# Performance work log

Measured on AMD Instinct MI355X. Metric: run time of the kernel, lower is better.

The kernel has to match this reference:

```python
import jax, jax.numpy as jnp
import numpy as np

B, C, D, H, W, K = 2, 192, 48, 48, 48, 7
EPS_LN = 1e-6
EPS_GRN = 1e-6


def setup_inputs() -> dict:
    key = jax.random.key(0)
    ks = jax.random.split(key, 8)
    sc = 0.02
    return {
        "x": jax.random.normal(ks[0], (B, C, D, H, W), jnp.float32),
        # depthwise conv kernel in DHWIO layout: [K,K,K,1,C] (torch weight [C,1,K,K,K])
        "conv_w": jax.random.normal(ks[1], (K, K, K, 1, C), jnp.float32) * sc,
        "conv_b": jnp.zeros((C,), jnp.float32),
        "ln_g": jnp.ones((C,), jnp.float32),
        "ln_b": jnp.zeros((C,), jnp.float32),
        "w1": jax.random.normal(ks[2], (C, 4 * C), jnp.float32) * sc,
        "b1": jnp.zeros((4 * C,), jnp.float32),
        "grn_gamma": jax.random.normal(ks[3], (4 * C,), jnp.float32) * sc,
        "grn_beta": jax.random.normal(ks[4], (4 * C,), jnp.float32) * sc,
        "w2": jax.random.normal(ks[5], (4 * C, C), jnp.float32) * sc,
        "b2": jnp.zeros((C,), jnp.float32),
    }


def reference(x, conv_w, conv_b, ln_g, ln_b, w1, b1, grn_gamma, grn_beta, w2, b2):
    c = x.shape[1]
    # NCDHW -> NDHWC (channels-last, as Permute([0,2,3,4,1]) after the conv)
    xc = jnp.transpose(x, (0, 2, 3, 4, 1))
    # depthwise conv3d, kernel 7, pad 3 (SAME for stride 1)
    y = jax.lax.conv_general_dilated(
        xc, conv_w, window_strides=(1, 1, 1), padding="SAME",
        dimension_numbers=("NDHWC", "DHWIO", "NDHWC"),
        feature_group_count=c,
    ) + conv_b
    # LayerNorm over channel dim, eps=1e-6 (biased variance, like torch)
    mu = jnp.mean(y, axis=-1, keepdims=True)
    var = jnp.mean(jnp.square(y - mu), axis=-1, keepdims=True)
    y = (y - mu) * jax.lax.rsqrt(var + EPS_LN) * ln_g + ln_b
    # MLP up + exact GELU
    y = jax.nn.gelu(y @ w1 + b1, approximate=False)
    # GRN: global L2 over spatial dims per channel
    gx = jnp.sqrt(jnp.sum(y * y, axis=(1, 2, 3), keepdims=True))  # [B,1,1,1,4C]
    nx = gx / (jnp.mean(gx, axis=-1, keepdims=True) + EPS_GRN)
    y = grn_gamma * (y * nx) + grn_beta + y
    # MLP down, permute back, residual
    y = y @ w2 + b2
    return jnp.transpose(y, (0, 4, 1, 2, 3)) + x
```

## Files before the change

### kernel.cpp

```cpp
#include <hip/hip_runtime.h>
#include <math.h>

#define Bn 2
#define Cn 192
#define Dn 48
#define Hn 48
#define Wn 48
#define C4 768
#define DHW (Dn*Hn*Wn)
#define CDHW ((long)Cn*DHW)

typedef __attribute__((ext_vector_type(8))) short bf16x8;
typedef __attribute__((ext_vector_type(4))) float f32x4;

__device__ inline float bf2f(unsigned short u) {
    union { float f; unsigned int i; } v; v.i = ((unsigned int)u) << 16; return v.f;
}
__device__ inline unsigned short f2bf(float f) {
    union { float f; unsigned int i; } v; v.f = f;
    unsigned int r = v.i + 0x7FFFu + ((v.i >> 16) & 1u);
    return (unsigned short)(r >> 16);
}
__device__ inline float blo(unsigned int u) {
    union { unsigned int i; float f; } v; v.i = u << 16; return v.f;
}
__device__ inline float bhi(unsigned int u) {
    union { unsigned int i; float f; } v; v.i = u & 0xffff0000u; return v.f;
}
__device__ inline unsigned int cvtpk_bf16(float lo, float hi) {
    unsigned int r;
    asm("v_cvt_pk_bf16_f32 %0, %1, %2" : "=v"(r) : "v"(lo), "v"(hi));
    return r;
}
__device__ inline float gelu_tanh(float v) {
    float u = v * fmaf(0.0356774081f, v * v, 0.7978845608f);
    float a = fabsf(u);
    float t = __expf(-2.0f * a);
    float th = (1.0f - t) / (1.0f + t);
    th = copysignf(th, u);
    return 0.5f * v * (1.0f + th);
}

__global__ __launch_bounds__(256)
void xpad_k(const float* __restrict__ x, unsigned short* __restrict__ xbf)
{
    int u = blockIdx.x * 256 + threadIdx.x;
    int j = u & 7;
    int row = u >> 3;
    unsigned short* orow = xbf + ((size_t)row << 6);
    uint4 o = {0u, 0u, 0u, 0u};
    if (j >= 1 && j <= 6) {
        const float* xr = x + (size_t)row * 48 + (8 * j - 8);
        float4 a = *(const float4*)xr;
        float4 b = *(const float4*)(xr + 4);
        o.x = cvtpk_bf16(a.x, a.y); o.y = cvtpk_bf16(a.z, a.w);
        o.z = cvtpk_bf16(b.x, b.y); o.w = cvtpk_bf16(b.z, b.w);
    }
    *(uint4*)(orow + 8 * j) = o;
}

__global__ __launch_bounds__(256)
void btoep_k(const float* __restrict__ cw, unsigned short* __restrict__ btp)
{
    int idx = blockIdx.x * 256 + threadIdx.x;
    int lane = idx & 63;
    int t = idx >> 6;
    int kdkh = t % 49, c = t / 49;
    int n = lane & 15, g = lane >> 4;
    unsigned short v[8];
#pragma unroll
    for (int j = 0; j < 8; ++j) {
        int kw = 8 * g + j - n - 5;
        v[j] = (kw >= 0 && kw <= 6) ? f2bf(cw[(kdkh * 7 + kw) * Cn + c])
                                    : (unsigned short)0;
    }
    *(uint4*)(btp + (size_t)idx * 8) = *(uint4*)v;
}

#define CTD 16
#define CHD (CTD+6)
#define CHH 22

__global__ __launch_bounds__(128)
void conv_dw(const unsigned short* __restrict__ xbf, const unsigned short* __restrict__ btp,
             const float* __restrict__ cb, unsigned short* __restrict__ yc)
{
    __shared__ unsigned int xt[CHD * CHH * 16];
    int c = blockIdx.y;
    int s = blockIdx.x;
    int wt = s % 3, ht = (s / 3) % 3, dt = s / 9;
    int d0 = dt * 16, h0 = ht * 16, w0 = wt * 16;
    int tid = threadIdx.x;

    const unsigned short* xc = xbf + ((size_t)c * 2304 << 6);
    for (int u = tid; u < CHD * CHH * 4; u += 128) {
        int g = u & 3, r2 = u >> 2;
        int hh2 = r2 % CHH, dd = r2 / CHH;
        int gd = d0 - 3 + dd, gh = h0 - 3 + hh2;
        uint4 v = {0u, 0u, 0u, 0u};
        if ((unsigned)gd < 48u && (unsigned)gh < 48u)
            v = *(const uint4*)(xc + (((size_t)gd * 48 + gh) << 6) + w0 + 8 * g);
        *(uint4*)&xt[(r2 << 4) + ((g ^ (r2 & 3)) << 2)] = v;
    }
    __syncthreads();

    int lane = tid & 63, wv = tid >> 6;
    int lr = lane & 15, g = lane >> 4;
    float bias = cb[c];
    f32x4 acc[8];
#pragma unroll
    for (int t = 0; t < 8; ++t) acc[t] = (f32x4){bias, bias, bias, bias};

    const unsigned short* bchan = btp + (size_t)c * 49 * 512;
    const unsigned short* xt16 = (const unsigned short*)xt;

    for (int kh = 0; kh < 7; ++kh) {
        bf16x8 Bf[7];
#pragma unroll
        for (int kd = 0; kd < 7; ++kd)
            Bf[kd] = *(const bf16x8*)(bchan + (size_t)((kd * 7 + kh) * 64 + lane) * 8);
#pragma unroll
        for (int p = 0; p < 14; ++p) {
            int r2 = (8 * wv + p) * CHH + kh + lr;
            bf16x8 Af = *(const bf16x8*)(xt16 + (r2 << 5) + ((g ^ (r2 & 3)) << 3));
#pragma unroll
            for (int kd = 0; kd < 7; ++kd) {
                int t = p - kd;
                if (t < 0 || t > 7) continue;
                acc[t] = __builtin_amdgcn_mfma_f32_16x16x32_bf16(Af, Bf[kd], acc[t], 0, 0, 0);
            }
        }
    }

    unsigned short* yb = yc + (long)c * DHW;
#pragma unroll
    for (int t = 0; t < 8; ++t) {
        int d = d0 + 8 * wv + t;
#pragma unroll
        for (int i = 0; i < 4; ++i) {
            int h = h0 + g * 4 + i;
            yb[((long)d * 48 + h) * 48 + w0 + lr] = f2bf(acc[t][i]);
        }
    }
}

__global__ __launch_bounds__(256)
void ln_kernel(const unsigned short* __restrict__ yc, const float* __restrict__ g,
               const float* __restrict__ lb, unsigned short* __restrict__ y1)
{
    __shared__ float tile[Cn * Wn];
    __shared__ float qs1[4][48], qs2[4][48];
    __shared__ float mu_s[Wn], rs_s[Wn];
    int dh = blockIdx.x;
    long rowbase = (long)dh * Wn;
    for (int l = threadIdx.x; l < Cn * 24; l += 256) {
        int c = l / 24, wp = l % 24;
        unsigned int u = *(const unsigned int*)&yc[rowbase + (long)c * DHW + wp * 2];
        tile[c * Wn + wp * 2]     = blo(u);
        tile[c * Wn + wp * 2 + 1] = bhi(u);
    }
    __syncthreads();
    if (threadIdx.x < 192) {
        int w = threadIdx.x >> 2, q = threadIdx.x & 3;
        float s1 = 0.f, s2 = 0.f;
        for (int cc = 0; cc < 48; ++cc) {
            float v = tile[(cc * 4 + q) * Wn + w];
            s1 += v; s2 = fmaf(v, v, s2);
        }
        qs1[q][w] = s1; qs2[q][w] = s2;
    }
    __syncthreads();
    if (threadIdx.x < 48) {
        int w = threadIdx.x;
        float s1 = qs1[0][w] + qs1[1][w] + qs1[2][w] + qs1[3][w];
        float s2 = qs2[0][w] + qs2[1][w] + qs2[2][w] + qs2[3][w];
        float mu = s1 * (1.0f / Cn);
        float var = s2 * (1.0f / Cn) - mu * mu;
        mu_s[w] = mu;
        rs_s[w] = rsqrtf(var + 1e-6f);
    }
    __syncthreads();
    long obase = (long)dh * Wn * Cn;
    for (int l = threadIdx.x; l < Cn * Wn; l += 256) {
        int w = l / Cn, c = l % Cn;
        float val = (tile[c * Wn + w] - mu_s[w]) * rs_s[w] * g[c] + lb[c];
        y1[obase + l] = f2bf(val);
    }
}

__global__ __launch_bounds__(256)
void wtrans(const float* __restrict__ W, unsigned short* __restrict__ Wt, int K, int N)
{
    int idx = blockIdx.x * 256 + threadIdx.x;
    if (idx >= K * N) return;
    int n = idx / K, k = idx % K;
    Wt[idx] = f2bf(W[(long)k * N + n]);
}

__global__ __launch_bounds__(256)
void wscale(const float* __restrict__ W2, const float* __restrict__ gx2,
            const float* __restrict__ gamma, unsigned short* __restrict__ W2s)
{
    __shared__ float red[256];
    int t = threadIdx.x;
    float s = 0.f;
#pragma unroll
    for (int i = 0; i < 3; ++i) s += sqrtf(gx2[t + i * 256]);
    red[t] = s; __syncthreads();
    for (int st = 128; st > 0; st >>= 1) {
        if (t < st) red[t] += red[t + st];
        __syncthreads();
    }
    float inv = 1.0f / (red[0] * (1.0f / C4) + 1e-6f);
    int idx = blockIdx.x * 256 + t;
    int n = idx / C4, k = idx % C4;
    float snx = 1.0f + gamma[k] * sqrtf(gx2[k]) * inv;
    W2s[idx] = f2bf(W2[(long)k * Cn + n] * snx);
}

__global__ __launch_bounds__(256)
void gemm_up(const unsigned short* __restrict__ A, const unsigned short* __restrict__ Bt,
             const float* __restrict__ bias, unsigned short* __restrict__ Y2,
             float* __restrict__ partial)
{
    __shared__ short Asm[128 * Cn];
    __shared__ float colsum[2][C4];
    int tid = threadIdx.x;
    int lane = tid & 63, wv = tid >> 6;
    int wm = wv >> 1, wn = wv & 1;
    int lr = lane & 15, lq = lane >> 4;
    long m0 = (long)blockIdx.x * 128;

#pragma unroll
    for (int i = 0; i < 12; ++i) {
        int chunk = i * 256 + tid;
        int r = chunk / 24, cc = chunk - r * 24;
        bf16x8 v = *(const bf16x8*)(A + (size_t)(m0 + r) * Cn + cc * 8);
        *(bf16x8*)&Asm[r * Cn + ((cc ^ (r & 7)) * 8)] = v;
    }
    __syncthreads();

    for (int nt = 0; nt < 12; ++nt) {
        int n0 = nt * 64;
        f32x4 acc[4][2];
#pragma unroll
        for (int mi = 0; mi < 4; ++mi)
#pragma unroll
            for (int ni = 0; ni < 2; ++ni) acc[mi][ni] = (f32x4){0.f, 0.f, 0.f, 0.f};

#pragma unroll
        for (int ks = 0; ks < 6; ++ks) {
            bf16x8 af[4], bfr[2];
#pragma unroll
            for (int ni = 0; ni < 2; ++ni) {
                int nrow = n0 + wn * 32 + ni * 16 + lr;
                bfr[ni] = *(const bf16x8*)(Bt + (size_t)nrow * Cn + (ks * 4 + lq) * 8);
            }
#pragma unroll
            for (int mi = 0; mi < 4; ++mi) {
                int r = wm * 64 + mi * 16 + lr;
                int cc = (ks * 4 + lq) ^ (r & 7);
                af[mi] = *(const bf16x8*)&Asm[r * Cn + cc * 8];
            }
#pragma unroll
            for (int mi = 0; mi < 4; ++mi)
#pragma unroll
                for (int ni = 0; ni < 2; ++ni)
                    acc[mi][ni] = __builtin_amdgcn_mfma_f32_16x16x32_bf16(
                        af[mi], bfr[ni], acc[mi][ni], 0, 0, 0);
        }

        float ss[2] = {0.f, 0.f};
#pragma unroll
        for (int mi = 0; mi < 4; ++mi) {
#pragma unroll
            for (int ni = 0; ni < 2; ++ni) {
                int col = wn * 32 + ni * 16 + lr;
                float bb = bias[n0 + col];
                long row0 = m0 + wm * 64 + mi * 16 + lq * 4;
#pragma unroll
                for (int i = 0; i < 4; ++i) {
                    float v = gelu_tanh(acc[mi][ni][i] + bb);
                    ss[ni] = fmaf(v, v, ss[ni]);
                    Y2[(row0 + i) * C4 + n0 + col] = f2bf(v);
                }
            }
        }
#pragma unroll
        for (int ni = 0; ni < 2; ++ni) {
            ss[ni] += __shfl_xor(ss[ni], 16);
            ss[ni] += __shfl_xor(ss[ni], 32);
        }
        if (lq == 0) {
            colsum[wm][n0 + wn * 32 + lr]      = ss[0];
            colsum[wm][n0 + wn * 32 + 16 + lr] = ss[1];
        }
    }
    __syncthreads();
    for (int i = tid; i < C4; i += 256)
        partial[(size_t)blockIdx.x * C4 + i] = colsum[0][i] + colsum[1][i];
}

__global__ __launch_bounds__(256)
void gemm_down(const unsigned short* __restrict__ A, const unsigned short* __restrict__ Bt,
               const float* __restrict__ beff, const float* __restrict__ x,
               float* __restrict__ out)
{
    __shared__ short Asm[128 * 64];
    int tid = threadIdx.x;
    int lane = tid & 63, wv = tid >> 6;
    int wm = wv >> 1, wn = wv & 1;
    int lr = lane & 15, lq = lane >> 4;
    long m0 = (long)blockIdx.x * 128;

    f32x4 acc[3][4][2];
#pragma unroll
    for (int nt = 0; nt < 3; ++nt)
#pragma unroll
        for (int mi = 0; mi < 4; ++mi)
#pragma unroll
            for (int ni = 0; ni < 2; ++ni) acc[nt][mi][ni] = (f32x4){0.f, 0.f, 0.f, 0.f};

    for (int k0 = 0; k0 < C4; k0 += 64) {
#pragma unroll
        for (int i = 0; i < 4; ++i) {
            int chunk = i * 256 + tid;
            int r = chunk >> 3, cc = chunk & 7;
            bf16x8 v = *(const bf16x8*)(A + (size_t)(m0 + r) * C4 + k0 + cc * 8);
            *(bf16x8*)&Asm[r * 64 + ((cc ^ (r & 7)) * 8)] = v;
        }
        __syncthreads();
#pragma unroll
        for (int ks = 0; ks < 2; ++ks) {
            bf16x8 af[4];
#pragma unroll
            for (int mi = 0; mi < 4; ++mi) {
                int r = wm * 64 + mi * 16 + lr;
                int cc = (ks * 4 + lq) ^ (r & 7);
                af[mi] = *(const bf16x8*)&Asm[r * 64 + cc * 8];
            }
#pragma unroll
            for (int nt = 0; nt < 3; ++nt) {
                bf16x8 bfr[2];
#pragma unroll
                for (int ni = 0; ni < 2; ++ni) {
                    int nrow = nt * 64 + wn * 32 + ni * 16 + lr;
                    bfr[ni] = *(const bf16x8*)(Bt + (size_t)nrow * C4 + k0 + (ks * 4 + lq) * 8);
                }
#pragma unroll
                for (int mi = 0; mi < 4; ++mi)
#pragma unroll
                    for (int ni = 0; ni < 2; ++ni)
                        acc[nt][mi][ni] = __builtin_amdgcn_mfma_f32_16x16x32_bf16(
                            af[mi], bfr[ni], acc[nt][mi][ni], 0, 0, 0);
            }
        }
        __syncthreads();
    }

#pragma unroll
    for (int nt = 0; nt < 3; ++nt) {
#pragma unroll
        for (int mi = 0; mi < 4; ++mi) {
#pragma unroll
            for (int ni = 0; ni < 2; ++ni) {
                int colg = nt * 64 + wn * 32 + ni * 16 + lr;
                float be = beff[colg];
                long mbase = m0 + wm * 64 + mi * 16 + lq * 4;
                const float* xp = x + (long)colg * DHW + mbase;
                float* op = out + (long)colg * DHW + mbase;
                float4 xvv = *(const float4*)xp;
                float4 o;
                o.x = acc[nt][mi][ni][0] + be + xvv.x;
                o.y = acc[nt][mi][ni][1] + be + xvv.y;
                o.z = acc[nt][mi][ni][2] + be + xvv.z;
                o.w = acc[nt][mi][ni][3] + be + xvv.w;
                *(float4*)op = o;
            }
        }
    }
}

__global__ __launch_bounds__(256)
void grn_reduce(const float* __restrict__ partial, float* __restrict__ gx2)
{
    int n = blockIdx.x;
    const float* p = partial + n;
    float s = 0.f;
    for (int r = threadIdx.x; r < 864; r += 256) s += p[(long)r * C4];
    __shared__ float red[256];
    red[threadIdx.x] = s; __syncthreads();
    for (int st = 128; st > 0; st >>= 1) {
        if (threadIdx.x < st) red[threadIdx.x] += red[threadIdx.x + st];
        __syncthreads();
    }
    if (threadIdx.x == 0) gx2[n] = red[0];
}

__global__ __launch_bounds__(256)
void bias_eff_k(const float* __restrict__ beta, const float* __restrict__ W2,
                const float* __restrict__ b2, float* __restrict__ beff)
{
    __shared__ float red[256];
    int j = blockIdx.x, t = threadIdx.x;
    float s = 0.f;
#pragma unroll
    for (int i = 0; i < 3; ++i) {
        int k = t + i * 256;
        s = fmaf(beta[k], W2[(long)k * Cn + j], s);
    }
    red[t] = s; __syncthreads();
    for (int st = 128; st > 0; st >>= 1) {
        if (t < st) red[t] += red[t + st];
        __syncthreads();
    }
    if (t == 0) beff[j] = red[0] + b2[j];
}

extern "C" void kernel_launch(void* const* d_in, const int* in_sizes, int n_in,
                              void* d_out, int out_size, void* d_ws, size_t ws_size,
                              hipStream_t stream) {
    const float* x      = (const float*)d_in[0];
    const float* conv_w = (const float*)d_in[1];
    const float* conv_b = (const float*)d_in[2];
    const float* ln_g   = (const float*)d_in[3];
    const float* ln_b   = (const float*)d_in[4];
    const float* w1     = (const float*)d_in[5];
    const float* b1     = (const float*)d_in[6];
    const float* gg     = (const float*)d_in[7];
    const float* gb     = (const float*)d_in[8];
    const float* w2     = (const float*)d_in[9];
    const float* b2     = (const float*)d_in[10];
    float* out = (float*)d_out;
    char* ws = (char*)d_ws;

    unsigned short* yc  = (unsigned short*)(ws);
    unsigned short* xbf = (unsigned short*)(ws + 42467328L);
    unsigned short* y2  = (unsigned short*)(ws);
    unsigned short* y1  = (unsigned short*)(ws + 169869312L);
    unsigned short* btp = (unsigned short*)(ws + 202702848L);
    float*     partial  = (float*)(ws + 212336640L);
    unsigned short* w1t = (unsigned short*)(ws + 214990848L);
    unsigned short* w2s = (unsigned short*)(ws + 215285760L);
    float*         gx2  = (float*)(ws + 215580672L);
    float*        beff  = (float*)(ws + 215586816L);

    bias_eff_k<<<Cn, 256, 0, stream>>>(gb, w2, b2, beff);
    wtrans<<<(Cn * C4 + 255) / 256, 256, 0, stream>>>(w1, w1t, Cn, C4);

    for (int b = 0; b < Bn; ++b) {
        const float* xb = x + (size_t)b * CDHW;
        float* outb = out + (size_t)b * CDHW;
        xpad_k<<<(Cn * 2304 * 8) / 256, 256, 0, stream>>>(xb, xbf);
        btoep_k<<<(Cn * 49 * 64) / 256, 256, 0, stream>>>(conv_w, btp);
        dim3 gc(27, Cn);
        conv_dw<<<gc, 128, 0, stream>>>(xbf, btp, conv_b, yc);
        ln_kernel<<<Dn * Hn, 256, 0, stream>>>(yc, ln_g, ln_b, y1);
        gemm_up<<<DHW / 128, 256, 0, stream>>>(y1, w1t, b1, y2, partial);
        grn_reduce<<<C4, 256, 0, stream>>>(partial, gx2);
        wscale<<<(Cn * C4) / 256, 256, 0, stream>>>(w2, gx2, gg, w2s);
        gemm_down<<<DHW / 128, 256, 0, stream>>>(y2, w2s, beff, xb, outb);
    }
}
```

Baseline: 858.6 us.

## Tile gemm_down over N with B staged in LDS, use fast reciprocal in GELU

gemm_down previously had each block cover all 192 output columns and read B fragments straight from global memory. It now launches a 2D grid with 64-column N tiles and stages both A and B into swizzled LDS. This cuts accumulator registers, which may raise occupancy, and triples the block count. The cost is that each A tile is reloaded three times, once per N tile, and the A loads are not prefetched. The GELU tanh division is also replaced with a hardware reciprocal multiply.

Measured after the change: 780.8 us, median of 2. 1.1x faster.

```diff
diff --git a/kernel.cpp b/kernel.cpp
--- a/kernel.cpp
+++ b/kernel.cpp
@@ -36,7 +36,7 @@
     float u = v * fmaf(0.0356774081f, v * v, 0.7978845608f);
     float a = fabsf(u);
     float t = __expf(-2.0f * a);
-    float th = (1.0f - t) / (1.0f + t);
+    float th = (1.0f - t) * __builtin_amdgcn_rcpf(1.0f + t);
     th = copysignf(th, u);
     return 0.5f * v * (1.0f + th);
 }
@@ -301,82 +301,87 @@
         partial[(size_t)blockIdx.x * C4 + i] = colsum[0][i] + colsum[1][i];
 }
 
+#define BM 128
+#define BN 64
+#define BK 64
+
 __global__ __launch_bounds__(256)
 void gemm_down(const unsigned short* __restrict__ A, const unsigned short* __restrict__ Bt,
                const float* __restrict__ beff, const float* __restrict__ x,
                float* __restrict__ out)
 {
-    __shared__ short Asm[128 * 64];
+    __shared__ short Asm[BM * BK];
+    __shared__ short Bsm[BN * BK];
     int tid = threadIdx.x;
     int lane = tid & 63, wv = tid >> 6;
     int wm = wv >> 1, wn = wv & 1;
     int lr = lane & 15, lq = lane >> 4;
-    long m0 = (long)blockIdx.x * 128;
-
-    f32x4 acc[3][4][2];
-#pragma unroll
-    for (int nt = 0; nt < 3; ++nt)
-#pragma unroll
-        for (int mi = 0; mi < 4; ++mi)
-#pragma unroll
-            for (int ni = 0; ni < 2; ++ni) acc[nt][mi][ni] = (f32x4){0.f, 0.f, 0.f, 0.f};
-
-    for (int k0 = 0; k0 < C4; k0 += 64) {
+    long m0 = (long)blockIdx.y * BM;
+    int n0 = blockIdx.x * BN;
+
+    f32x4 acc[4][2];
+#pragma unroll
+    for (int mi = 0; mi < 4; ++mi)
+#pragma unroll
+        for (int ni = 0; ni < 2; ++ni) acc[mi][ni] = (f32x4){0.f, 0.f, 0.f, 0.f};
+
+    for (int k0 = 0; k0 < C4; k0 += BK) {
 #pragma unroll
         for (int i = 0; i < 4; ++i) {
             int chunk = i * 256 + tid;
             int r = chunk >> 3, cc = chunk & 7;
             bf16x8 v = *(const bf16x8*)(A + (size_t)(m0 + r) * C4 + k0 + cc * 8);
-            *(bf16x8*)&Asm[r * 64 + ((cc ^ (r & 7)) * 8)] = v;
+            *(bf16x8*)&Asm[r * BK + ((cc ^ (r & 7)) * 8)] = v;
+        }
+#pragma unroll
+        for (int i = 0; i < 2; ++i) {
+            int chunk = i * 256 + tid;
+            int r = chunk >> 3, cc = chunk & 7;
+            bf16x8 v = *(const bf16x8*)(Bt + (size_t)(n0 + r) * C4 + k0 + cc * 8);
+            *(bf16x8*)&Bsm[r * BK + ((cc ^ (r & 7)) * 8)] = v;
         }
         __syncthreads();
 #pragma unroll
-        for (int ks = 0; ks < 2; ++ks) {
-            bf16x8 af[4];
+        for (int kk = 0; kk < 2; ++kk) {
+            bf16x8 af[4], bfr[2];
 #pragma unroll
             for (int mi = 0; mi < 4; ++mi) {
                 int r = wm * 64 + mi * 16 + lr;
-                int cc = (ks * 4 + lq) ^ (r & 7);
-                af[mi] = *(const bf16x8*)&Asm[r * 64 + cc * 8];
-            }
-#pragma unroll
-            for (int nt = 0; nt < 3; ++nt) {
-                bf16x8 bfr[2];
-#pragma unroll
-                for (int ni = 0; ni < 2; ++ni) {
-                    int nrow = nt * 64 + wn * 32 + ni * 16 + lr;
-                    bfr[ni] = *(const bf16x8*)(Bt + (size_t)nrow * C4 + k0 + (ks * 4 + lq) * 8);
-                }
-#pragma unroll
-                for (int mi = 0; mi < 4; ++mi)
-#pragma unroll
-                    for (int ni = 0; ni < 2; ++ni)
-                        acc[nt][mi][ni] = __builtin_amdgcn_mfma_f32_16x16x32_bf16(
-                            af[mi], bfr[ni], acc[nt][mi][ni], 0, 0, 0);
-            }
+                int cc = (kk * 4 + lq) ^ (r & 7);
+                af[mi] = *(const bf16x8*)&Asm[r * BK + cc * 8];
+            }
+#pragma unroll
+            for (int ni = 0; ni < 2; ++ni) {
+                int r = wn * 32 + ni * 16 + lr;
+                int cc = (kk * 4 + lq) ^ (r & 7);
+                bfr[ni] = *(const bf16x8*)&Bsm[r * BK + cc * 8];
+            }
+#pragma unroll
+            for (int mi = 0; mi < 4; ++mi)
+#pragma unroll
+                for (int ni = 0; ni < 2; ++ni)
+                    acc[mi][ni] = __builtin_amdgcn_mfma_f32_16x16x32_bf16(
+                        af[mi], bfr[ni], acc[mi][ni], 0, 0, 0);
         }
         __syncthreads();
     }
 
 #pragma unroll
-    for (int nt = 0; nt < 3; ++nt) {
-#pragma unroll
-        for (int mi = 0; mi < 4; ++mi) {
-#pragma unroll
-            for (int ni = 0; ni < 2; ++ni) {
-                int colg = nt * 64 + wn * 32 + ni * 16 + lr;
-                float be = beff[colg];
-                long mbase = m0 + wm * 64 + mi * 16 + lq * 4;
-                const float* xp = x + (long)colg * DHW + mbase;
-                float* op = out + (long)colg * DHW + mbase;
-                float4 xvv = *(const float4*)xp;
-                float4 o;
-                o.x = acc[nt][mi][ni][0] + be + xvv.x;
-                o.y = acc[nt][mi][ni][1] + be + xvv.y;
-                o.z = acc[nt][mi][ni][2] + be + xvv.z;
-                o.w = acc[nt][mi][ni][3] + be + xvv.w;
-                *(float4*)op = o;
-            }
+    for (int mi = 0; mi < 4; ++mi) {
+#pragma unroll
+        for (int ni = 0; ni < 2; ++ni) {
+            int colg = n0 + wn * 32 + ni * 16 + lr;
+            float be = beff[colg];
+            long mbase = m0 + wm * 64 + mi * 16 + lq * 4;
+            const float* xp = x + (long)colg * DHW + mbase;
+            float* op = out + (long)colg * DHW + mbase;
+            float4 xvv = *(const float4*)xp;
+            float4 o;
+            o.x = acc[mi][ni][0] + be + xvv.x;
+            o.y = acc[mi][ni][1] + be + xvv.y;
+            o.z = acc[mi][ni][2] + be + xvv.z;
+            o.w = acc[mi][ni][3] + be + xvv.w;
+            *(float4*)op = o;
         }
     }
 }
@@ -459,6 +464,7 @@
         gemm_up<<<DHW / 128, 256, 0, stream>>>(y1, w1t, b1, y2, partial);
         grn_reduce<<<C4, 256, 0, stream>>>(partial, gx2);
         wscale<<<(Cn * C4) / 256, 256, 0, stream>>>(w2, gx2, gg, w2s);
-        gemm_down<<<DHW / 128, 256, 0, stream>>>(y2, w2s, beff, xb, outb);
-    }
-}
+        dim3 gd(Cn / BN, DHW / BM);
+        gemm_down<<<gd, 256, 0, stream>>>(y2, w2s, beff, xb, outb);
+    }
+}
```
